# Kernel tuning notes

Measured on AMD Instinct MI355X. Metric: run time of the kernel, lower is better.

Reference implementation:

```python
import jax, jax.numpy as jnp
import numpy as np

# Config constants (match init_kwargs / config)
B = 16        # config.BATCH_SIZE
T = 2048      # config.TRAIN_LEN
C = 256       # input channels (input_shape[-1])
K = 8         # kernel_size
F = 256       # nb_filters
DIL = 4       # dilation_rate


def setup_inputs() -> dict:
    key = jax.random.key(0)
    k1, k2, k3 = jax.random.split(key, 3)
    inputs = jax.random.normal(k1, (B, T, C), dtype=jnp.float32)
    kernel = jax.random.normal(k2, (C, K, F), dtype=jnp.float32) * 0.05
    bias = jax.random.normal(k3, (F,), dtype=jnp.float32) * 0.05
    return {"inputs": inputs, "kernel": kernel, "bias": bias}


def reference(inputs, kernel, bias):
    # Original TF layer computes, per (b,t,k,f):
    #   raw[b,t,k,f] = sum_c (x[b,t,c] * kernel[c,k,f] + bias[f])
    #               = conv[b,t,k,f] + C * bias[f]
    # (bias is added BEFORE the reduce_sum over the channel axis, so it is
    #  scaled by C — we reproduce that quirk faithfully.)
    # Then each (t,k) slice is scatter-added to output time t + k*dilation
    # (the gather_nd + zero-pad construction in TF implements exactly this
    #  dilated transposed-conv scatter; non-matching positions gather zeros),
    # and finally the last T timesteps are kept.
    Bq, Tq, Cq = inputs.shape
    Kq, Fq = kernel.shape[1], kernel.shape[2]
    conv = jnp.einsum('btc,ckf->btkf', inputs, kernel) + jnp.asarray(Cq, inputs.dtype) * bias
    L = Tq + (Kq - 1) * DIL  # final_time_len
    # scatter positions: out[i + j*DIL] += conv[:, i, j, :]
    pos = (jnp.arange(Tq)[:, None] + DIL * jnp.arange(Kq)[None, :]).reshape(-1)  # (T*K,)
    out = jnp.zeros((Bq, L, Fq), dtype=conv.dtype)
    out = out.at[:, pos, :].add(conv.reshape(Bq, Tq * Kq, Fq))
    return out[:, -Tq:, :]
```

## Files before the change

### kernel.cpp

```cpp
#include <hip/hip_runtime.h>
#include <hip/hip_bf16.h>


#define B_   16
#define T_   2048
#define C_   256
#define KT   8
#define F_   256
#define SH   28
#define BT   128
#define WIN  156
#define TPAD 192
#define TILEB (TPAD * 64)

typedef __attribute__((ext_vector_type(8))) short short8;
typedef __attribute__((ext_vector_type(4))) float floatx4;
typedef __attribute__((ext_vector_type(4))) int   intx4;

__global__ __launch_bounds__(256) void wprep_kernel(const float* __restrict__ W,
                                                    ushort* __restrict__ Wf) {
    const int tid  = threadIdx.x;
    const int fid  = blockIdx.x * 4 + (tid >> 6);
    const int lane = tid & 63;
    const int g    = fid & 15;
    const int S    = fid >> 4;
    const int j    = S & 7, c = S >> 3;
    const int c0   = c * 32 + (lane >> 4) * 8;
    const int f    = g * 16 + (lane & 15);
    short8 pk;
    #pragma unroll
    for (int i = 0; i < 8; ++i) {
        __hip_bfloat16 h = __float2bfloat16(W[((c0 + i) * KT + j) * F_ + f]);
        pk[i] = *reinterpret_cast<const short*>(&h);
    }
    *reinterpret_cast<short8*>(Wf + (size_t)fid * 512 + lane * 8) = pk;
}

__device__ inline short8 cvt8v(floatx4 a, floatx4 b) {
    short8 r;
    #pragma unroll
    for (int i = 0; i < 4; ++i) {
        __hip_bfloat16 h = __float2bfloat16(a[i]);
        r[i] = *reinterpret_cast<const short*>(&h);
    }
    #pragma unroll
    for (int i = 0; i < 4; ++i) {
        __hip_bfloat16 h = __float2bfloat16(b[i]);
        r[i + 4] = *reinterpret_cast<const short*>(&h);
    }
    return r;
}

__global__ __launch_bounds__(256, 2) void deconv_kernel(
        const float* __restrict__ x, const ushort* __restrict__ Wf,
        const float* __restrict__ bias, float* __restrict__ out) {
    __shared__ alignas(16) char smem[2 * TILEB];
    const int bid = blockIdx.x;
    const int fh  = bid & 1;
    const int tb  = bid >> 1;
    const int b   = tb & 15;
    const int t0  = (tb >> 4) * BT;
    const int tid = threadIdx.x;
    const int w   = tid >> 6, lane = tid & 63;
    const int l16 = lane & 15, q = lane >> 4;
    const int wm  = w >> 1, wf2 = w & 1;
    const char* wfbase = (const char*)Wf +
        (size_t)(fh * 8 + wf2 * 4) * 1024 + (size_t)lane * 16;
    const int srow = tid >> 2, sg = tid & 3;

#define VMW(N_) do { asm volatile("s_waitcnt vmcnt(" #N_ ")" ::: "memory"); \
        __builtin_amdgcn_sched_barrier(0); } while (0)
#define LKW() do { asm volatile("s_waitcnt lgkmcnt(0)" ::: "memory");       \
        __builtin_amdgcn_sched_barrier(0); } while (0)
#define BAR() do { __builtin_amdgcn_sched_barrier(0);                       \
        __builtin_amdgcn_s_barrier();                                       \
        asm volatile("" ::: "memory");                                      \
        __builtin_amdgcn_sched_barrier(0); } while (0)

#define SL_ISSUE(cs_) do {                                                  \
        _Pragma("unroll")                                                   \
        for (int k = 0; k < 3; ++k) {                                       \
            int tr_ = t0 + srow + 64 * k;                                   \
            if (tr_ > T_ - 1) tr_ = T_ - 1;                                 \
            const char* p_ = (const char*)(x +                              \
                ((size_t)(b * T_ + tr_) * C_ + (cs_) * 32 + sg * 8));       \
            asm volatile("global_load_dwordx4 %0, %1, off"                  \
                : "=v"(sl[k][0]) : "v"(p_) : "memory");                     \
            asm volatile("global_load_dwordx4 %0, %1, off offset:16"        \
                : "=v"(sl[k][1]) : "v"(p_) : "memory");                     \
        } } while (0)

#define CVT_WRITE(buf_) do {                                                \
        _Pragma("unroll")                                                   \
        for (int k = 0; k < 3; ++k) {                                       \
            const int row_ = srow + 64 * k;                                 \
            short8 pk_ = {0,0,0,0,0,0,0,0};                                 \
            if (t0 + row_ < T_) pk_ = cvt8v(sl[k][0], sl[k][1]);            \
            const int p_ = sg ^ ((row_ >> 1) & 3);                          \
            *(short8*)(smem + (buf_) * TILEB + row_ * 64 + p_ * 16) = pk_;  \
        } } while (0)

#define A_LOAD(buf_) do {                                                   \
        _Pragma("unroll")                                                   \
        for (int d = 0; d < 20; ++d) {                                      \
            const int row_ = wm * 64 + l16 + 4 * d;                         \
            const int p_   = q ^ ((row_ >> 1) & 3);                         \
            a[d] = *(const short8*)(smem + (buf_) * TILEB +                 \
                                    row_ * 64 + p_ * 16);                   \
        } } while (0)

#define B_ISSUE(S_, sl_) do {                                               \
        const char* p_ = wfbase + (size_t)(S_) * 16384;                     \
        asm volatile("global_load_dwordx4 %0, %1, off"                      \
            : "=v"(bR[sl_][0]) : "v"(p_) : "memory");                       \
        asm volatile("global_load_dwordx4 %0, %1, off offset:1024"          \
            : "=v"(bR[sl_][1]) : "v"(p_) : "memory");                       \
        asm volatile("global_load_dwordx4 %0, %1, off offset:2048"          \
            : "=v"(bR[sl_][2]) : "v"(p_) : "memory");                       \
        asm volatile("global_load_dwordx4 %0, %1, off offset:3072"          \
            : "=v"(bR[sl_][3]) : "v"(p_) : "memory");                       \
        } while (0)

#define MFMA_TAP(j_, slot_) do {                                            \
        __builtin_amdgcn_s_setprio(1);                                      \
        _Pragma("unroll")                                                   \
        for (int mf = 0; mf < 4; ++mf)                                      \
            _Pragma("unroll")                                               \
            for (int nf = 0; nf < 4; ++nf)                                  \
                acc[mf][nf] = __builtin_amdgcn_mfma_f32_16x16x32_bf16(      \
                    a[7 - (j_) + 4 * mf],                                   \
                    *(short8*)&bR[slot_][nf],                               \
                    acc[mf][nf], 0, 0, 0);                                  \
        __builtin_amdgcn_s_setprio(0);                                      \
        } while (0)

#define CHUNK(c_) do {                                                      \
        A_LOAD((c_) & 1);                                                   \
        B_ISSUE((c_)*8+2, (((c_)*8+2)%3)); VMW(8);                          \
        MFMA_TAP(0, (((c_)*8+0)%3));                                        \
        B_ISSUE((c_)*8+3, (((c_)*8+3)%3)); VMW(8);                          \
        MFMA_TAP(1, (((c_)*8+1)%3));                                        \
        SL_ISSUE((c_) + 1);                                                 \
        B_ISSUE((c_)*8+4, (((c_)*8+4)%3)); VMW(14);                         \
        MFMA_TAP(2, (((c_)*8+2)%3));                                        \
        B_ISSUE((c_)*8+5, (((c_)*8+5)%3)); VMW(14);                         \
        MFMA_TAP(3, (((c_)*8+3)%3));                                        \
        B_ISSUE((c_)*8+6, (((c_)*8+6)%3)); VMW(8);                          \
        MFMA_TAP(4, (((c_)*8+4)%3));                                        \
        B_ISSUE((c_)*8+7, (((c_)*8+7)%3)); VMW(8);                          \
        MFMA_TAP(5, (((c_)*8+5)%3));                                        \
        CVT_WRITE(((c_) + 1) & 1);                                          \
        B_ISSUE((c_)*8+8, (((c_)*8+8)%3)); VMW(8);                          \
        MFMA_TAP(6, (((c_)*8+6)%3));                                        \
        B_ISSUE((c_)*8+9, (((c_)*8+9)%3)); VMW(8);                          \
        MFMA_TAP(7, (((c_)*8+7)%3));                                        \
        LKW(); BAR();                                                       \
        } while (0)

    float bf4[4];
    #pragma unroll
    for (int nf = 0; nf < 4; ++nf)
        bf4[nf] = bias[fh * 128 + wf2 * 64 + nf * 16 + l16];

    floatx4 acc[4][4];
    #pragma unroll
    for (int mf = 0; mf < 4; ++mf)
        #pragma unroll
        for (int nf = 0; nf < 4; ++nf)
            acc[mf][nf] = (floatx4){0.f, 0.f, 0.f, 0.f};

    short8  a[20];
    intx4   bR[3][4];
    floatx4 sl[3][2];

    SL_ISSUE(0);
    B_ISSUE(0, 0); B_ISSUE(1, 1);
    VMW(8);
    CVT_WRITE(0);
    LKW(); BAR();

    CHUNK(0); CHUNK(1); CHUNK(2); CHUNK(3);
    CHUNK(4); CHUNK(5); CHUNK(6);

    A_LOAD(1);
    B_ISSUE(58, 1); VMW(8); MFMA_TAP(0, 2);
    B_ISSUE(59, 2); VMW(8); MFMA_TAP(1, 0);
    B_ISSUE(60, 0); VMW(8); MFMA_TAP(2, 1);
    B_ISSUE(61, 1); VMW(8); MFMA_TAP(3, 2);
    B_ISSUE(62, 2); VMW(8); MFMA_TAP(4, 0);
    B_ISSUE(63, 0); VMW(8); MFMA_TAP(5, 1);
    VMW(4); MFMA_TAP(6, 2);
    VMW(0); MFMA_TAP(7, 0);

    #pragma unroll
    for (int mf = 0; mf < 4; ++mf) {
        #pragma unroll
        for (int nf = 0; nf < 4; ++nf) {
            const int f = fh * 128 + wf2 * 64 + nf * 16 + l16;
            #pragma unroll
            for (int r = 0; r < 4; ++r) {
                const int t = t0 + wm * 64 + mf * 16 + q * 4 + r;
                const int jmin = (t < T_ - SH) ? 0 : (((t - (T_ - SH)) >> 2) + 1);
                out[(size_t)(b * T_ + t) * F_ + f] =
                    acc[mf][nf][r] + (float)(8 - jmin) * 256.0f * bf4[nf];
            }
        }
    }
#undef VMW
#undef LKW
#undef BAR
#undef SL_ISSUE
#undef CVT_WRITE
#undef A_LOAD
#undef B_ISSUE
#undef MFMA_TAP
#undef CHUNK
}

extern "C" void kernel_launch(void* const* d_in, const int* in_sizes, int n_in,
                              void* d_out, int out_size, void* d_ws, size_t ws_size,
                              hipStream_t stream) {
    const float* x    = (const float*)d_in[0];
    const float* W    = (const float*)d_in[1];
    const float* bias = (const float*)d_in[2];
    float* out = (float*)d_out;
    ushort* Wf = (ushort*)d_ws;

    wprep_kernel<<<256, 256, 0, stream>>>(W, Wf);
    deconv_kernel<<<512, 256, 0, stream>>>(x, Wf, bias, out);
}
```

Measured before the change: 49.85 us.

## Switch to 32x32x16 MFMA with per-tap LDS A loads and deeper x prefetch

Replaces the 16x16x32 bf16 MFMA tiling with 32x32x16 MFMAs and re-lays out the prepared weight fragments to match. Instead of holding 20 A fragments in registers for a whole chunk, it loads A fragments from LDS for each tap with ping-pong register sets, and trims the LDS tile to the 156 rows actually needed. The x prefetch now runs two chunks ahead, and the LDS writes are split into rounds interleaved with the MFMAs. The aim is fewer MFMA issues and lower register pressure, at the cost of more LDS reads per tap and dropping the two-blocks-per-CU launch bound.

Result: faster. 47.77 us (-4.2%).

```diff
diff --git a/kernel.cpp b/kernel.cpp
--- a/kernel.cpp
+++ b/kernel.cpp
@@ -9,12 +9,11 @@
 #define F_   256
 #define SH   28
 #define BT   128
-#define WIN  156
-#define TPAD 192
-#define TILEB (TPAD * 64)
+#define ABFB 9984
 
 typedef __attribute__((ext_vector_type(8))) short short8;
 typedef __attribute__((ext_vector_type(4))) float floatx4;
+typedef __attribute__((ext_vector_type(16))) float floatx16;
 typedef __attribute__((ext_vector_type(4))) int   intx4;
 
 __global__ __launch_bounds__(256) void wprep_kernel(const float* __restrict__ W,
@@ -22,16 +21,18 @@
     const int tid  = threadIdx.x;
     const int fid  = blockIdx.x * 4 + (tid >> 6);
     const int lane = tid & 63;
-    const int g    = fid & 15;
-    const int S    = fid >> 4;
-    const int j    = S & 7, c = S >> 3;
-    const int c0   = c * 32 + (lane >> 4) * 8;
-    const int f    = g * 16 + (lane & 15);
+    const int l5 = lane & 31, h = lane >> 5;
+    const int knf = fid & 3, kh = knf >> 1, nf = knf & 1;
+    const int fqg = (fid >> 2) & 3;
+    const int S   = fid >> 4;
+    const int j   = S & 7, ch = S >> 3;
+    const int c0  = ch * 32 + kh * 16 + h * 8;
+    const int f   = fqg * 64 + nf * 32 + l5;
     short8 pk;
     #pragma unroll
     for (int i = 0; i < 8; ++i) {
-        __hip_bfloat16 h = __float2bfloat16(W[((c0 + i) * KT + j) * F_ + f]);
-        pk[i] = *reinterpret_cast<const short*>(&h);
+        __hip_bfloat16 v = __float2bfloat16(W[((c0 + i) * KT + j) * F_ + f]);
+        pk[i] = *reinterpret_cast<const short*>(&v);
     }
     *reinterpret_cast<short8*>(Wf + (size_t)fid * 512 + lane * 8) = pk;
 }
@@ -51,10 +52,10 @@
     return r;
 }
 
-__global__ __launch_bounds__(256, 2) void deconv_kernel(
+__global__ __launch_bounds__(256) void deconv_kernel(
         const float* __restrict__ x, const ushort* __restrict__ Wf,
         const float* __restrict__ bias, float* __restrict__ out) {
-    __shared__ alignas(16) char smem[2 * TILEB];
+    __shared__ alignas(16) char smem[2 * ABFB];
     const int bid = blockIdx.x;
     const int fh  = bid & 1;
     const int tb  = bid >> 1;
@@ -62,10 +63,10 @@
     const int t0  = (tb >> 4) * BT;
     const int tid = threadIdx.x;
     const int w   = tid >> 6, lane = tid & 63;
-    const int l16 = lane & 15, q = lane >> 4;
-    const int wm  = w >> 1, wf2 = w & 1;
+    const int l5  = lane & 31, h = lane >> 5;
+    const int wm  = w >> 1, fq2 = w & 1;
     const char* wfbase = (const char*)Wf +
-        (size_t)(fh * 8 + wf2 * 4) * 1024 + (size_t)lane * 16;
+        (size_t)(fh * 2 + fq2) * 4096 + (size_t)lane * 16;
     const int srow = tid >> 2, sg = tid & 3;
 
 #define VMW(N_) do { asm volatile("s_waitcnt vmcnt(" #N_ ")" ::: "memory"); \
@@ -77,36 +78,26 @@
         asm volatile("" ::: "memory");                                      \
         __builtin_amdgcn_sched_barrier(0); } while (0)
 
-#define SL_ISSUE(cs_) do {                                                  \
+#define SL_ISSUE(cc_) do {                                                  \
         _Pragma("unroll")                                                   \
         for (int k = 0; k < 3; ++k) {                                       \
-            int tr_ = t0 + srow + 64 * k;                                   \
-            if (tr_ > T_ - 1) tr_ = T_ - 1;                                 \
+            int row_ = srow + 64 * k;                                       \
+            int tr_ = t0 + row_; if (tr_ > T_ - 1) tr_ = T_ - 1;            \
             const char* p_ = (const char*)(x +                              \
-                ((size_t)(b * T_ + tr_) * C_ + (cs_) * 32 + sg * 8));       \
+                ((size_t)(b * T_ + tr_) * C_ + (cc_) * 32 + sg * 8));       \
             asm volatile("global_load_dwordx4 %0, %1, off"                  \
                 : "=v"(sl[k][0]) : "v"(p_) : "memory");                     \
             asm volatile("global_load_dwordx4 %0, %1, off offset:16"        \
                 : "=v"(sl[k][1]) : "v"(p_) : "memory");                     \
         } } while (0)
 
-#define CVT_WRITE(buf_) do {                                                \
-        _Pragma("unroll")                                                   \
-        for (int k = 0; k < 3; ++k) {                                       \
-            const int row_ = srow + 64 * k;                                 \
+#define WR_ROUND(k_, buf_) do {                                             \
+        const int row_ = srow + 64 * (k_);                                  \
+        if (row_ < 156) {                                                   \
             short8 pk_ = {0,0,0,0,0,0,0,0};                                 \
-            if (t0 + row_ < T_) pk_ = cvt8v(sl[k][0], sl[k][1]);            \
+            if (t0 + row_ < T_) pk_ = cvt8v(sl[k_][0], sl[k_][1]);          \
             const int p_ = sg ^ ((row_ >> 1) & 3);                          \
-            *(short8*)(smem + (buf_) * TILEB + row_ * 64 + p_ * 16) = pk_;  \
-        } } while (0)
-
-#define A_LOAD(buf_) do {                                                   \
-        _Pragma("unroll")                                                   \
-        for (int d = 0; d < 20; ++d) {                                      \
-            const int row_ = wm * 64 + l16 + 4 * d;                         \
-            const int p_   = q ^ ((row_ >> 1) & 3);                         \
-            a[d] = *(const short8*)(smem + (buf_) * TILEB +                 \
-                                    row_ * 64 + p_ * 16);                   \
+            *(short8*)(smem + (buf_) * ABFB + row_ * 64 + p_ * 16) = pk_;   \
         } } while (0)
 
 #define B_ISSUE(S_, sl_) do {                                               \
@@ -121,88 +112,127 @@
             : "=v"(bR[sl_][3]) : "v"(p_) : "memory");                       \
         } while (0)
 
-#define MFMA_TAP(j_, slot_) do {                                            \
+#define LOAD_A(buf_, j_, arr) do {                                          \
+        const char* ab_ = smem + (buf_) * ABFB;                             \
+        _Pragma("unroll")                                                   \
+        for (int kh = 0; kh < 2; ++kh)                                      \
+            _Pragma("unroll")                                               \
+            for (int mf = 0; mf < 2; ++mf) {                                \
+                const int row_ = wm * 64 + (SH - 4 * (j_)) + mf * 32 + l5;  \
+                const int p_ = (kh * 2 + h) ^ ((row_ >> 1) & 3);            \
+                arr[kh * 2 + mf] = *(const short8*)(ab_ + row_ * 64 +       \
+                                                    p_ * 16);               \
+            } } while (0)
+
+#define MFMA_TAP(arr, slot_) do {                                           \
         __builtin_amdgcn_s_setprio(1);                                      \
         _Pragma("unroll")                                                   \
-        for (int mf = 0; mf < 4; ++mf)                                      \
+        for (int mf = 0; mf < 2; ++mf)                                      \
             _Pragma("unroll")                                               \
-            for (int nf = 0; nf < 4; ++nf)                                  \
-                acc[mf][nf] = __builtin_amdgcn_mfma_f32_16x16x32_bf16(      \
-                    a[7 - (j_) + 4 * mf],                                   \
-                    *(short8*)&bR[slot_][nf],                               \
+            for (int nf = 0; nf < 2; ++nf) {                                \
+                acc[mf][nf] = __builtin_amdgcn_mfma_f32_32x32x16_bf16(      \
+                    arr[0 * 2 + mf], *(short8*)&bR[slot_][0 * 2 + nf],      \
                     acc[mf][nf], 0, 0, 0);                                  \
+                acc[mf][nf] = __builtin_amdgcn_mfma_f32_32x32x16_bf16(      \
+                    arr[1 * 2 + mf], *(short8*)&bR[slot_][1 * 2 + nf],      \
+                    acc[mf][nf], 0, 0, 0);                                  \
+            }                                                               \
         __builtin_amdgcn_s_setprio(0);                                      \
         } while (0)
 
-#define CHUNK(c_) do {                                                      \
-        A_LOAD((c_) & 1);                                                   \
-        B_ISSUE((c_)*8+2, (((c_)*8+2)%3)); VMW(8);                          \
-        MFMA_TAP(0, (((c_)*8+0)%3));                                        \
-        B_ISSUE((c_)*8+3, (((c_)*8+3)%3)); VMW(8);                          \
-        MFMA_TAP(1, (((c_)*8+1)%3));                                        \
-        SL_ISSUE((c_) + 1);                                                 \
-        B_ISSUE((c_)*8+4, (((c_)*8+4)%3)); VMW(14);                         \
-        MFMA_TAP(2, (((c_)*8+2)%3));                                        \
-        B_ISSUE((c_)*8+5, (((c_)*8+5)%3)); VMW(14);                         \
-        MFMA_TAP(3, (((c_)*8+3)%3));                                        \
+#define CHUNK_STEADY(c_, DOSL_) do {                                        \
+        const int bf_ = (c_) & 1;                                           \
+        LOAD_A(bf_, 0, aA); LOAD_A(bf_, 1, aB);                             \
+        B_ISSUE((c_)*8+2, (((c_)*8+2)%3)); VMW(14);                         \
+        MFMA_TAP(aA, (((c_)*8+0)%3)); LOAD_A(bf_, 2, aA);                   \
+        B_ISSUE((c_)*8+3, (((c_)*8+3)%3)); VMW(14);                         \
+        MFMA_TAP(aB, (((c_)*8+1)%3)); LOAD_A(bf_, 3, aB);                   \
+        B_ISSUE((c_)*8+4, (((c_)*8+4)%3)); VMW(8);                          \
+        MFMA_TAP(aA, (((c_)*8+2)%3)); LOAD_A(bf_, 4, aA);                   \
+        B_ISSUE((c_)*8+5, (((c_)*8+5)%3)); VMW(8);                          \
+        MFMA_TAP(aB, (((c_)*8+3)%3)); LOAD_A(bf_, 5, aB);                   \
+        WR_ROUND(0, bf_ ^ 1);                                               \
         B_ISSUE((c_)*8+6, (((c_)*8+6)%3)); VMW(8);                          \
-        MFMA_TAP(4, (((c_)*8+4)%3));                                        \
+        MFMA_TAP(aA, (((c_)*8+4)%3)); LOAD_A(bf_, 6, aA);                   \
+        WR_ROUND(1, bf_ ^ 1);                                               \
         B_ISSUE((c_)*8+7, (((c_)*8+7)%3)); VMW(8);                          \
-        MFMA_TAP(5, (((c_)*8+5)%3));                                        \
-        CVT_WRITE(((c_) + 1) & 1);                                          \
+        MFMA_TAP(aB, (((c_)*8+5)%3)); LOAD_A(bf_, 7, aB);                   \
+        WR_ROUND(2, bf_ ^ 1);                                               \
         B_ISSUE((c_)*8+8, (((c_)*8+8)%3)); VMW(8);                          \
-        MFMA_TAP(6, (((c_)*8+6)%3));                                        \
+        MFMA_TAP(aA, (((c_)*8+6)%3));                                       \
         B_ISSUE((c_)*8+9, (((c_)*8+9)%3)); VMW(8);                          \
-        MFMA_TAP(7, (((c_)*8+7)%3));                                        \
+        MFMA_TAP(aB, (((c_)*8+7)%3));                                       \
+        if (DOSL_) SL_ISSUE((c_) + 2);                                      \
         LKW(); BAR();                                                       \
         } while (0)
 
-    float bf4[4];
-    #pragma unroll
-    for (int nf = 0; nf < 4; ++nf)
-        bf4[nf] = bias[fh * 128 + wf2 * 64 + nf * 16 + l16];
-
-    floatx4 acc[4][4];
-    #pragma unroll
-    for (int mf = 0; mf < 4; ++mf)
+    float bf2[2];
+    bf2[0] = bias[fh * 128 + fq2 * 64 + l5];
+    bf2[1] = bias[fh * 128 + fq2 * 64 + 32 + l5];
+
+    floatx16 acc[2][2];
+    #pragma unroll
+    for (int mf = 0; mf < 2; ++mf)
         #pragma unroll
-        for (int nf = 0; nf < 4; ++nf)
-            acc[mf][nf] = (floatx4){0.f, 0.f, 0.f, 0.f};
-
-    short8  a[20];
+        for (int nf = 0; nf < 2; ++nf)
+            #pragma unroll
+            for (int r = 0; r < 16; ++r) acc[mf][nf][r] = 0.f;
+
+    short8  aA[4], aB[4];
     intx4   bR[3][4];
     floatx4 sl[3][2];
 
     SL_ISSUE(0);
+    VMW(0);
+    WR_ROUND(0, 0); WR_ROUND(1, 0); WR_ROUND(2, 0);
+    SL_ISSUE(1);
     B_ISSUE(0, 0); B_ISSUE(1, 1);
-    VMW(8);
-    CVT_WRITE(0);
     LKW(); BAR();
 
-    CHUNK(0); CHUNK(1); CHUNK(2); CHUNK(3);
-    CHUNK(4); CHUNK(5); CHUNK(6);
-
-    A_LOAD(1);
-    B_ISSUE(58, 1); VMW(8); MFMA_TAP(0, 2);
-    B_ISSUE(59, 2); VMW(8); MFMA_TAP(1, 0);
-    B_ISSUE(60, 0); VMW(8); MFMA_TAP(2, 1);
-    B_ISSUE(61, 1); VMW(8); MFMA_TAP(3, 2);
-    B_ISSUE(62, 2); VMW(8); MFMA_TAP(4, 0);
-    B_ISSUE(63, 0); VMW(8); MFMA_TAP(5, 1);
-    VMW(4); MFMA_TAP(6, 2);
-    VMW(0); MFMA_TAP(7, 0);
-
-    #pragma unroll
-    for (int mf = 0; mf < 4; ++mf) {
+    {
+        LOAD_A(0, 0, aA); LOAD_A(0, 1, aB);
+        B_ISSUE(2, 2);  VMW(8); MFMA_TAP(aA, 0); LOAD_A(0, 2, aA);
+        B_ISSUE(3, 0);  VMW(8); MFMA_TAP(aB, 1); LOAD_A(0, 3, aB);
+        B_ISSUE(4, 1);  VMW(8); MFMA_TAP(aA, 2); LOAD_A(0, 4, aA);
+        B_ISSUE(5, 2);  VMW(8); MFMA_TAP(aB, 0); LOAD_A(0, 5, aB);
+        WR_ROUND(0, 1);
+        B_ISSUE(6, 0);  VMW(8); MFMA_TAP(aA, 1); LOAD_A(0, 6, aA);
+        WR_ROUND(1, 1);
+        B_ISSUE(7, 1);  VMW(8); MFMA_TAP(aB, 2); LOAD_A(0, 7, aB);
+        WR_ROUND(2, 1);
+        B_ISSUE(8, 2);  VMW(8); MFMA_TAP(aA, 0);
+        B_ISSUE(9, 0);  VMW(8); MFMA_TAP(aB, 1);
+        SL_ISSUE(2);
+        LKW(); BAR();
+    }
+
+    CHUNK_STEADY(1, 1); CHUNK_STEADY(2, 1); CHUNK_STEADY(3, 1);
+    CHUNK_STEADY(4, 1); CHUNK_STEADY(5, 1); CHUNK_STEADY(6, 0);
+
+    {
+        LOAD_A(1, 0, aA); LOAD_A(1, 1, aB);
+        B_ISSUE(58, 1); VMW(8); MFMA_TAP(aA, 2); LOAD_A(1, 2, aA);
+        B_ISSUE(59, 2); VMW(8); MFMA_TAP(aB, 0); LOAD_A(1, 3, aB);
+        B_ISSUE(60, 0); VMW(8); MFMA_TAP(aA, 1); LOAD_A(1, 4, aA);
+        B_ISSUE(61, 1); VMW(8); MFMA_TAP(aB, 2); LOAD_A(1, 5, aB);
+        B_ISSUE(62, 2); VMW(8); MFMA_TAP(aA, 0); LOAD_A(1, 6, aA);
+        B_ISSUE(63, 0); VMW(8); MFMA_TAP(aB, 1); LOAD_A(1, 7, aB);
+        VMW(4); MFMA_TAP(aA, 2);
+        VMW(0); MFMA_TAP(aB, 0);
+    }
+
+    #pragma unroll
+    for (int mf = 0; mf < 2; ++mf) {
         #pragma unroll
-        for (int nf = 0; nf < 4; ++nf) {
-            const int f = fh * 128 + wf2 * 64 + nf * 16 + l16;
+        for (int nf = 0; nf < 2; ++nf) {
+            const int f = fh * 128 + fq2 * 64 + nf * 32 + l5;
             #pragma unroll
-            for (int r = 0; r < 4; ++r) {
-                const int t = t0 + wm * 64 + mf * 16 + q * 4 + r;
+            for (int r = 0; r < 16; ++r) {
+                const int rowin = (r & 3) + 8 * (r >> 2) + 4 * h;
+                const int t = t0 + wm * 64 + mf * 32 + rowin;
                 const int jmin = (t < T_ - SH) ? 0 : (((t - (T_ - SH)) >> 2) + 1);
                 out[(size_t)(b * T_ + t) * F_ + f] =
-                    acc[mf][nf][r] + (float)(8 - jmin) * 256.0f * bf4[nf];
+                    acc[mf][nf][r] + (float)(8 - jmin) * 256.0f * bf2[nf];
             }
         }
     }
@@ -210,11 +240,11 @@
 #undef LKW
 #undef BAR
 #undef SL_ISSUE
-#undef CVT_WRITE
-#undef A_LOAD
+#undef WR_ROUND
 #undef B_ISSUE
+#undef LOAD_A
 #undef MFMA_TAP
-#undef CHUNK
+#undef CHUNK_STEADY
 }
 
 extern "C" void kernel_launch(void* const* d_in, const int* in_sizes, int n_in,
```
